# Kernel tuning notes

Hardware: AMD Instinct MI355X
Metric: run time of the kernel (lower is better)

## Reference

```python
import jax, jax.numpy as jnp
import numpy as np

N, D, H, E = 50000, 64, 4, 400000
LN_EPS = 1e-5


def setup_inputs() -> dict:
    key = jax.random.key(0)
    ks = jax.random.split(key, 8)
    x = jax.random.normal(ks[0], (N, D), dtype=jnp.float32)
    edge_index = jax.random.randint(ks[1], (2, E), 0, N, dtype=jnp.int64)
    # nn.Linear(dim, dim*heads, bias=False): weight shape (H*D, D)
    W_lin = jax.random.normal(ks[2], (H * D, D), dtype=jnp.float32) * (1.0 / np.sqrt(D))
    attn_src = jax.random.normal(ks[3], (H, D), dtype=jnp.float32) * 0.1
    attn_dst = jax.random.normal(ks[4], (H, D), dtype=jnp.float32) * 0.1
    # nn.Linear(dim*heads, dim): weight (D, H*D), bias (D,)
    W_out = jax.random.normal(ks[5], (D, H * D), dtype=jnp.float32) * (1.0 / np.sqrt(H * D))
    b_out = jnp.zeros((D,), dtype=jnp.float32)
    ln_g = jnp.ones((D,), dtype=jnp.float32)
    ln_b = jnp.zeros((D,), dtype=jnp.float32)
    return {"x": x, "edge_index": edge_index, "W_lin": W_lin,
            "attn_src": attn_src, "attn_dst": attn_dst,
            "W_out": W_out, "b_out": b_out, "ln_g": ln_g, "ln_b": ln_b}


def reference(x, edge_index, W_lin, attn_src, attn_dst, W_out, b_out, ln_g, ln_b):
    n = x.shape[0]
    i, j = edge_index[0], edge_index[1]  # dst, src node ids per edge
    xh = (x @ W_lin.T).reshape(n, H, D)                 # [N,H,D]
    # per-node attention contributions (equivalent to per-edge dot in source)
    s_dst = jnp.einsum('nhd,hd->nh', xh, attn_dst)      # [N,H]
    s_src = jnp.einsum('nhd,hd->nh', xh, attn_src)      # [N,H]
    alpha = jax.nn.leaky_relu(s_dst[i] + s_src[j], 0.2) # [E,H]
    alpha_exp = jnp.exp(alpha)                          # source uses raw exp (no max-shift)
    denom = jax.ops.segment_sum(alpha_exp, i, num_segments=n)  # [N,H]
    attn = alpha_exp / (denom[i] + 1e-9)                # [E,H]
    msg = attn[:, :, None] * xh[j]                      # [E,H,D]
    out = jax.ops.segment_sum(msg, i, num_segments=n)   # [N,H,D]
    out = out.reshape(n, H * D) @ W_out.T + b_out       # [N,D]
    y = jax.nn.elu(out) + x
    mu = jnp.mean(y, axis=-1, keepdims=True)
    var = jnp.mean(jnp.square(y - mu), axis=-1, keepdims=True)
    return (y - mu) * jax.lax.rsqrt(var + LN_EPS) * ln_g + ln_b
```

## Files before the change

kernel.cpp:

```cpp
#include <hip/hip_runtime.h>

#define N_NODES 50000
#define DIM     64
#define HEADS   4
#define NEDGES  400000
#define HD      256
#define MAXDEG  32
#define NPREP   256
#define ZSTRIDE 264

#define USE_DOT2 1

typedef _Float16 half2v __attribute__((ext_vector_type(2)));
typedef _Float16 half4v __attribute__((ext_vector_type(4)));
typedef _Float16 half8v __attribute__((ext_vector_type(8)));
typedef float    f32x4  __attribute__((ext_vector_type(4)));

union EU { int2 i2; half4v h; };
union HU { unsigned int u; half2v h; };

__device__ __forceinline__ half2v h2cast(unsigned int u) { HU c; c.u = u; return c.h; }

#if USE_DOT2
#define DOT2(a, b, c) __builtin_amdgcn_fdot2((a), (b), (c), false)
#else
__device__ __forceinline__ float DOT2(half2v a, half2v b, float c) {
    return fmaf((float)a[1], (float)b[1], fmaf((float)a[0], (float)b[0], c));
}
#endif

__global__ __launch_bounds__(256) void k_prep(
    const float* __restrict__ x,
    const float* __restrict__ W_lin,
    const float* __restrict__ attn_src,
    const float* __restrict__ attn_dst,
    const float* __restrict__ W_out,
    const int* __restrict__ ei,
    _Float16* __restrict__ G2T,
    _Float16* __restrict__ x16,
    float* __restrict__ S,
    int* __restrict__ cnt,
    int* __restrict__ bucketJ)
{
    __shared__ float weffsh[512];
    const int b = blockIdx.x, t = threadIdx.x;

    for (int e = b * 256 + t; e < NEDGES; e += NPREP * 256) {
        const int i = ei[e];
        const int j = ei[NEDGES + e];
        const int slot = atomicAdd(&cnt[i], 1);
        if (slot < MAXDEG) bucketJ[(size_t)i * MAXDEG + slot] = j;
    }

    for (int id = t; id < 512; id += 256) {
        const int sd = id >> 8, rem = id & 255, h = rem >> 6, k = rem & 63;
        const float* av = sd ? attn_dst : attn_src;
        float acc = 0.f;
        for (int d = 0; d < DIM; ++d)
            acc = fmaf(av[h * DIM + d], W_lin[(h * DIM + d) * DIM + k], acc);
        weffsh[id] = acc;
    }

    {
        const int id = b * 256 + t;
        if (id < 64 * 256) {
            const int d = id >> 8, rem = id & 255, m = rem >> 2, h = rem & 3;
            float acc = 0.f;
            for (int k = 0; k < DIM; ++k)
                acc = fmaf(W_lin[(h * DIM + k) * DIM + m],
                           W_out[d * HD + h * DIM + k], acc);
            G2T[d * HD + m * 4 + h] = (_Float16)acc;
        }
    }
    __syncthreads();

    for (int base = b * 32; base < N_NODES; base += NPREP * 32) {
        const int ni = base + (t >> 3);
        if (ni < N_NODES) {
            const int combo = t & 7;
            const float4* xr = (const float4*)(x + (size_t)ni * DIM);
            const float4* wr = (const float4*)(weffsh + combo * DIM);
            float acc = 0.f;
#pragma unroll
            for (int kp = 0; kp < 16; ++kp) {
                const float4 a = xr[kp], bw = wr[kp];
                acc = fmaf(a.x, bw.x, acc);
                acc = fmaf(a.y, bw.y, acc);
                acc = fmaf(a.z, bw.z, acc);
                acc = fmaf(a.w, bw.w, acc);
            }
            S[(size_t)ni * 8 + combo] = acc;
        }
        const size_t e0 = (size_t)base * DIM + (size_t)t * 8;
        if (e0 + 8 <= (size_t)N_NODES * DIM) {
            const float4 u = *(const float4*)(x + e0);
            const float4 v = *(const float4*)(x + e0 + 4);
            half8v hv;
            hv[0]=(_Float16)u.x; hv[1]=(_Float16)u.y; hv[2]=(_Float16)u.z; hv[3]=(_Float16)u.w;
            hv[4]=(_Float16)v.x; hv[5]=(_Float16)v.y; hv[6]=(_Float16)v.z; hv[7]=(_Float16)v.w;
            *(half8v*)(x16 + e0) = hv;
        }
    }
}

__global__ __launch_bounds__(256) void k_ga(
    const int* __restrict__ cnt,
    const int* __restrict__ bucketJ,
    const float* __restrict__ S,
    const _Float16* __restrict__ x16,
    const _Float16* __restrict__ G2T,
    const float* __restrict__ b_out,
    const float* __restrict__ ln_g,
    const float* __restrict__ ln_b,
    float* __restrict__ out)
{
    __shared__ _Float16 znsh[16 * ZSTRIDE];
    __shared__ float ysh[16][65];
    __shared__ int2  esh[16 * 32];

    const int t = threadIdx.x, wv = t >> 6, l = t & 63;
    const int n0 = blockIdx.x * 16;
    const int side = l >> 5, p = l & 31;

    const int4 degv = *(const int4*)(cnt + n0 + wv * 4);
    int degc[4];
    degc[0] = degv.x < MAXDEG ? degv.x : MAXDEG;
    degc[1] = degv.y < MAXDEG ? degv.y : MAXDEG;
    degc[2] = degv.z < MAXDEG ? degv.z : MAXDEG;
    degc[3] = degv.w < MAXDEG ? degv.w : MAXDEG;

    int Jr[4];
#pragma unroll
    for (int r = 0; r < 4; ++r)
        Jr[r] = bucketJ[(unsigned)(n0 + wv * 4 + r) * MAXDEG + p];
#pragma unroll
    for (int r = 0; r < 4; ++r)
        Jr[r] = (p < degc[r]) ? Jr[r] : 0;

    float4 SSr[4], SDr[4];
#pragma unroll
    for (int r = 0; r < 4; ++r)
        SSr[r] = *(const float4*)(S + (unsigned)Jr[r] * 8);
#pragma unroll
    for (int r = 0; r < 4; ++r)
        SDr[r] = *(const float4*)(S + (unsigned)(n0 + wv * 4 + r) * 8 + 4);

#pragma unroll
    for (int r = 0; r < 4; ++r) {
        float u;
        u = SDr[r].x + SSr[r].x; u = u > 0.f ? u : 0.2f * u; const float e0 = __expf(u);
        u = SDr[r].y + SSr[r].y; u = u > 0.f ? u : 0.2f * u; const float e1 = __expf(u);
        u = SDr[r].z + SSr[r].z; u = u > 0.f ? u : 0.2f * u; const float e2 = __expf(u);
        u = SDr[r].w + SSr[r].w; u = u > 0.f ? u : 0.2f * u; const float e3 = __expf(u);
        EU pk;
        pk.h[0] = (_Float16)e0; pk.h[1] = (_Float16)e1;
        pk.h[2] = (_Float16)e2; pk.h[3] = (_Float16)e3;
        int2 ev = pk.i2;
        if (p >= degc[r]) { ev.x = 0; ev.y = 0; }
        if (side == 0) esh[(wv * 4 + r) * 32 + p] = ev;
    }
    __builtin_amdgcn_wave_barrier();

    struct Grp { half2v xv[4]; int2 ee[4]; };
    float za[4], zb[4], dd[4];
    const half2v one2 = h2cast(0x3C003C00u);

    auto stage_group = [&](int r, int s, Grp& g) {
        const int jb = s + side;
#pragma unroll
        for (int q = 0; q < 4; ++q) {
            const int jv = __shfl(Jr[r], jb + 2 * q, 64);
            g.xv[q] = *(const half2v*)(x16 + (unsigned)jv * DIM + (p << 1));
        }
        const int eb = (wv * 4 + r) * 32 + jb;
#pragma unroll
        for (int q = 0; q < 4; ++q)
            g.ee[q] = esh[eb + 2 * q];
    };

    auto consume_group = [&](const Grp& g) {
#pragma unroll
        for (int pp = 0; pp < 2; ++pp) {
            const int2 ea = g.ee[2 * pp], eb2 = g.ee[2 * pp + 1];
            HU xa, xb; xa.h = g.xv[2 * pp]; xb.h = g.xv[2 * pp + 1];
            const unsigned E0 = __builtin_amdgcn_perm(eb2.x, ea.x, 0x05040100u);
            const unsigned E1 = __builtin_amdgcn_perm(eb2.x, ea.x, 0x07060302u);
            const unsigned E2 = __builtin_amdgcn_perm(eb2.y, ea.y, 0x05040100u);
            const unsigned E3 = __builtin_amdgcn_perm(eb2.y, ea.y, 0x07060302u);
            const unsigned XA = __builtin_amdgcn_perm(xb.u, xa.u, 0x05040100u);
            const unsigned XB = __builtin_amdgcn_perm(xb.u, xa.u, 0x07060302u);
            const half2v f0 = h2cast(E0), f1 = h2cast(E1);
            const half2v f2 = h2cast(E2), f3 = h2cast(E3);
            const half2v va = h2cast(XA), vb = h2cast(XB);
            za[0] = DOT2(f0, va, za[0]); za[1] = DOT2(f1, va, za[1]);
            za[2] = DOT2(f2, va, za[2]); za[3] = DOT2(f3, va, za[3]);
            zb[0] = DOT2(f0, vb, zb[0]); zb[1] = DOT2(f1, vb, zb[1]);
            zb[2] = DOT2(f2, vb, zb[2]); zb[3] = DOT2(f3, vb, zb[3]);
            dd[0] = DOT2(f0, one2, dd[0]); dd[1] = DOT2(f1, one2, dd[1]);
            dd[2] = DOT2(f2, one2, dd[2]); dd[3] = DOT2(f3, one2, dd[3]);
        }
    };

    Grp cur, nxt, remb;
    stage_group(0, 0, cur);

#pragma unroll
    for (int r = 0; r < 4; ++r) {
        const bool rem = degc[r] > 8;
        if (rem) stage_group(r, 8, remb);
        if (r < 3) stage_group(r + 1, 0, nxt);

#pragma unroll
        for (int h = 0; h < 4; ++h) { za[h] = 0.f; zb[h] = 0.f; dd[h] = 0.f; }

        consume_group(cur);
        if (rem) {
            consume_group(remb);
            for (int s = 16; s < degc[r]; s += 8) {
                Grp tg;
                stage_group(r, s, tg);
                consume_group(tg);
            }
        }

#pragma unroll
        for (int h = 0; h < 4; ++h) {
            dd[h] += __shfl_xor(dd[h], 32, 64);
            za[h] += __shfl_xor(za[h], 32, 64);
            zb[h] += __shfl_xor(zb[h], 32, 64);
        }
        const float r0 = __builtin_amdgcn_rcpf(dd[0] + 1e-9f);
        const float r1 = __builtin_amdgcn_rcpf(dd[1] + 1e-9f);
        const float r2 = __builtin_amdgcn_rcpf(dd[2] + 1e-9f);
        const float r3 = __builtin_amdgcn_rcpf(dd[3] + 1e-9f);
        if (side == 0) {
            half8v o;
            o[0] = (_Float16)(za[0] * r0); o[1] = (_Float16)(za[1] * r1);
            o[2] = (_Float16)(za[2] * r2); o[3] = (_Float16)(za[3] * r3);
            o[4] = (_Float16)(zb[0] * r0); o[5] = (_Float16)(zb[1] * r1);
            o[6] = (_Float16)(zb[2] * r2); o[7] = (_Float16)(zb[3] * r3);
            *(half8v*)(znsh + (wv * 4 + r) * ZSTRIDE + p * 8) = o;
        }
        cur = nxt;
    }
    __syncthreads();

    const int mrow = l & 15, quad = l >> 4;
    half8v A[8];
    const _Float16* zr = znsh + mrow * ZSTRIDE + quad * 8;
#pragma unroll
    for (int s = 0; s < 8; ++s)
        A[s] = *(const half8v*)(zr + 32 * s);

    const _Float16* gp = G2T + (size_t)(wv * 16 + mrow) * HD + quad * 8;
    f32x4 c = {0.f, 0.f, 0.f, 0.f};
#pragma unroll
    for (int s = 0; s < 8; ++s)
        c = __builtin_amdgcn_mfma_f32_16x16x32_f16(A[s], *(const half8v*)(gp + 32 * s), c, 0, 0, 0);

    const int col = wv * 16 + mrow;
    const float bo = b_out[col];
#pragma unroll
    for (int rho = 0; rho < 4; ++rho) {
        const int nl = quad * 4 + rho;
        const float o = c[rho] + bo;
        const float eo = o > 0.f ? o : expm1f(o);
        ysh[nl][col] = eo + (float)x16[(size_t)(n0 + nl) * DIM + col];
    }
    __syncthreads();

    const float g = ln_g[l], bb = ln_b[l];
#pragma unroll
    for (int r = 0; r < 4; ++r) {
        const int nl = wv * 4 + r;
        const float y = ysh[nl][l];
        float sum = y;
#pragma unroll
        for (int off = 32; off > 0; off >>= 1) sum += __shfl_xor(sum, off, 64);
        const float mu = sum * (1.f / 64.f);
        const float dy = y - mu;
        float vs = dy * dy;
#pragma unroll
        for (int off = 32; off > 0; off >>= 1) vs += __shfl_xor(vs, off, 64);
        const float rr = rsqrtf(vs * (1.f / 64.f) + 1e-5f);
        out[(size_t)(n0 + nl) * DIM + l] = dy * rr * g + bb;
    }
}

extern "C" void kernel_launch(void* const* d_in, const int* in_sizes, int n_in,
                              void* d_out, int out_size, void* d_ws, size_t ws_size,
                              hipStream_t stream)
{
    const float* x        = (const float*)d_in[0];
    const int*   ei       = (const int*)d_in[1];
    const float* W_lin    = (const float*)d_in[2];
    const float* attn_src = (const float*)d_in[3];
    const float* attn_dst = (const float*)d_in[4];
    const float* W_out    = (const float*)d_in[5];
    const float* b_out    = (const float*)d_in[6];
    const float* ln_g     = (const float*)d_in[7];
    const float* ln_b     = (const float*)d_in[8];
    float* out = (float*)d_out;

    char* ws = (char*)d_ws;
    _Float16* x16    = (_Float16*)ws;
    float*    S      = (float*)(x16 + (size_t)N_NODES * DIM);
    _Float16* G2T    = (_Float16*)(S + (size_t)N_NODES * 8);
    int*      cnt    = (int*)(G2T + 64 * HD);
    int*      bucketJ= cnt + N_NODES;

    hipMemsetAsync(cnt, 0, (size_t)N_NODES * sizeof(int), stream);

    k_prep<<<NPREP, 256, 0, stream>>>(x, W_lin, attn_src, attn_dst, W_out, ei,
                                      G2T, x16, S, cnt, bucketJ);

    k_ga<<<N_NODES / 16, 256, 0, stream>>>(cnt, bucketJ, S, x16, G2T,
                                           b_out, ln_g, ln_b, out);
}
```

Before: 149.6 us.

## Prefetch neighbor feature gathers two rows ahead, hoisted before score computation

Separates x-feature gathering from attention-weight reads and issues neighbor gathers for rows r+1 and r+2, plus the remainder group of the next row, before the current row is consumed. The first gathers now start before the per-edge exp/score computation, so global-load latency overlaps the ALU work. NPREP is also raised from 256 to 1024, which changes the prep kernel's launch configuration. The trade-off is more live registers per thread, which can lower occupancy.

```diff
diff --git a/kernel.cpp b/kernel.cpp
--- a/kernel.cpp
+++ b/kernel.cpp
@@ -6,7 +6,7 @@
 #define NEDGES  400000
 #define HD      256
 #define MAXDEG  32
-#define NPREP   256
+#define NPREP   1024
 #define ZSTRIDE 264
 
 #define USE_DOT2 1
@@ -137,6 +137,22 @@
     for (int r = 0; r < 4; ++r)
         Jr[r] = (p < degc[r]) ? Jr[r] : 0;
 
+    auto stage_x = [&](int r, int s, half2v* xv) {
+        const int jb = s + side;
+        int jq[4];
+#pragma unroll
+        for (int q = 0; q < 4; ++q)
+            jq[q] = __shfl(Jr[r], jb + 2 * q, 64);
+#pragma unroll
+        for (int q = 0; q < 4; ++q)
+            xv[q] = *(const half2v*)(x16 + (unsigned)jq[q] * DIM + (p << 1));
+    };
+
+    half2v xcur[4], xnxt[4], xrem[4];
+    stage_x(0, 0, xcur);
+    if (degc[0] > 8) stage_x(0, 8, xrem);
+    stage_x(1, 0, xnxt);
+
     float4 SSr[4], SDr[4];
 #pragma unroll
     for (int r = 0; r < 4; ++r)
@@ -161,28 +177,21 @@
     }
     __builtin_amdgcn_wave_barrier();
 
-    struct Grp { half2v xv[4]; int2 ee[4]; };
+    auto read_e = [&](int r, int s, int2* ee) {
+        const int eb = (wv * 4 + r) * 32 + s + side;
+#pragma unroll
+        for (int q = 0; q < 4; ++q)
+            ee[q] = esh[eb + 2 * q];
+    };
+
     float za[4], zb[4], dd[4];
     const half2v one2 = h2cast(0x3C003C00u);
 
-    auto stage_group = [&](int r, int s, Grp& g) {
-        const int jb = s + side;
-#pragma unroll
-        for (int q = 0; q < 4; ++q) {
-            const int jv = __shfl(Jr[r], jb + 2 * q, 64);
-            g.xv[q] = *(const half2v*)(x16 + (unsigned)jv * DIM + (p << 1));
-        }
-        const int eb = (wv * 4 + r) * 32 + jb;
-#pragma unroll
-        for (int q = 0; q < 4; ++q)
-            g.ee[q] = esh[eb + 2 * q];
-    };
-
-    auto consume_group = [&](const Grp& g) {
+    auto consume = [&](const int2* ee, const half2v* xv) {
 #pragma unroll
         for (int pp = 0; pp < 2; ++pp) {
-            const int2 ea = g.ee[2 * pp], eb2 = g.ee[2 * pp + 1];
-            HU xa, xb; xa.h = g.xv[2 * pp]; xb.h = g.xv[2 * pp + 1];
+            const int2 ea = ee[2 * pp], eb2 = ee[2 * pp + 1];
+            HU xa, xb; xa.h = xv[2 * pp]; xb.h = xv[2 * pp + 1];
             const unsigned E0 = __builtin_amdgcn_perm(eb2.x, ea.x, 0x05040100u);
             const unsigned E1 = __builtin_amdgcn_perm(eb2.x, ea.x, 0x07060302u);
             const unsigned E2 = __builtin_amdgcn_perm(eb2.y, ea.y, 0x05040100u);
@@ -201,25 +210,28 @@
         }
     };
 
-    Grp cur, nxt, remb;
-    stage_group(0, 0, cur);
-
 #pragma unroll
     for (int r = 0; r < 4; ++r) {
-        const bool rem = degc[r] > 8;
-        if (rem) stage_group(r, 8, remb);
-        if (r < 3) stage_group(r + 1, 0, nxt);
+        const bool remc = degc[r] > 8;
+        half2v xnrem[4], xfar[4];
+        if (r < 3 && degc[r + 1] > 8) stage_x(r + 1, 8, xnrem);
+        if (r < 2) stage_x(r + 2, 0, xfar);
+
+        int2 ecur[4], erem[4];
+        read_e(r, 0, ecur);
+        if (remc) read_e(r, 8, erem);
 
 #pragma unroll
         for (int h = 0; h < 4; ++h) { za[h] = 0.f; zb[h] = 0.f; dd[h] = 0.f; }
 
-        consume_group(cur);
-        if (rem) {
-            consume_group(remb);
+        consume(ecur, xcur);
+        if (remc) {
+            consume(erem, xrem);
             for (int s = 16; s < degc[r]; s += 8) {
-                Grp tg;
-                stage_group(r, s, tg);
-                consume_group(tg);
+                half2v xt[4]; int2 et[4];
+                stage_x(r, s, xt);
+                read_e(r, s, et);
+                consume(et, xt);
             }
         }
 
@@ -241,7 +253,13 @@
             o[6] = (_Float16)(zb[2] * r2); o[7] = (_Float16)(zb[3] * r3);
             *(half8v*)(znsh + (wv * 4 + r) * ZSTRIDE + p * 8) = o;
         }
-        cur = nxt;
+
+#pragma unroll
+        for (int q = 0; q < 4; ++q) {
+            xcur[q] = xnxt[q];
+            xnxt[q] = xfar[q];
+            xrem[q] = xnrem[q];
+        }
     }
     __syncthreads();
 
```

Result: no change. 150.7 us (+0.7%).
